# Performance work log

Measured on AMD Instinct MI355X. Metric: run time of the kernel, lower is better.

Reference implementation:

```python
import jax, jax.numpy as jnp
import numpy as np

NHEAD = 16

def setup_inputs() -> dict:
    key = jax.random.key(0)
    ks = jax.random.split(key, 5)
    B, S, D = 4, 2048, 1024
    x = jax.random.normal(ks[0], (B, S, D), dtype=jnp.float32)
    in_proj_weight = jax.random.normal(ks[1], (3 * D, D), dtype=jnp.float32) * (D ** -0.5)
    in_proj_bias = jax.random.normal(ks[2], (3 * D,), dtype=jnp.float32) * 0.02
    out_w = jax.random.normal(ks[3], (D, D), dtype=jnp.float32) * (D ** -0.5)
    out_b = jax.random.normal(ks[4], (D,), dtype=jnp.float32) * 0.02
    return {"x": x, "in_proj_weight": in_proj_weight, "in_proj_bias": in_proj_bias,
            "out_w": out_w, "out_b": out_b}

def reference(x, in_proj_weight, in_proj_bias, out_w, out_b):
    # Faithful to nn.MultiheadAttention self-attn (prefill path, no mask).
    B, S, D = x.shape
    H = NHEAD
    hd = D // H
    qkv = x @ in_proj_weight.T + in_proj_bias            # [B,S,3D]
    q, k, v = jnp.split(qkv, 3, axis=-1)                 # each [B,S,D]
    def heads(t):
        return t.reshape(B, S, H, hd).transpose(0, 2, 1, 3)  # [B,H,S,hd]
    q, k, v = heads(q), heads(k), heads(v)
    scale = hd ** -0.5
    scores = jnp.einsum('bhqd,bhkd->bhqk', q * scale, k)  # [B,H,S,S]
    attn = jax.nn.softmax(scores, axis=-1)
    o = jnp.einsum('bhqk,bhkd->bhqd', attn, v)            # [B,H,S,hd]
    o = o.transpose(0, 2, 1, 3).reshape(B, S, D)
    return o @ out_w.T + out_b
```

## Files before the change

kernel.cpp:

```cpp
#include <hip/hip_runtime.h>
#include <hip/hip_bf16.h>
#include <math.h>

typedef __bf16 bf16_t;
typedef __bf16 bf16x8 __attribute__((ext_vector_type(8)));
typedef float  f32x4  __attribute__((ext_vector_type(4)));

#define DEV __device__ __forceinline__

#define BSZ    4
#define SEQ    2048
#define DMODEL 1024
#define NHEADS 16
#define HDIM   64
#define MROWS  (BSZ*SEQ)
#define KDIM   1024
#define NQKV   (3*DMODEL)

#define GLOAD_LDS16(src, dst)                                                  \
  __builtin_amdgcn_global_load_lds(                                            \
      (__attribute__((address_space(1))) void*)(void*)(src),                   \
      (__attribute__((address_space(3))) void*)(dst), 16, 0, 0)

DEV unsigned cvtpk_bf16(float lo, float hi) {
  unsigned r;
  asm("v_cvt_pk_bf16_f32 %0, %1, %2" : "=v"(r) : "v"(lo), "v"(hi));
  return r;
}

__global__ void cast3_f32_to_bf16(const float* __restrict__ a, int na4,
                                  const float* __restrict__ b, int nb4,
                                  const float* __restrict__ c, int nc4,
                                  bf16_t* __restrict__ oa,
                                  bf16_t* __restrict__ ob,
                                  bf16_t* __restrict__ oc) {
  union U { bf16_t h[4]; uint2 u; };
  int total = na4 + nb4 + nc4;
  for (int i = blockIdx.x * blockDim.x + threadIdx.x; i < total;
       i += gridDim.x * blockDim.x) {
    const float* src; bf16_t* dst; int k;
    if (i < na4)            { src = a; dst = oa; k = i; }
    else if (i < na4 + nb4) { src = b; dst = ob; k = i - na4; }
    else                    { src = c; dst = oc; k = i - na4 - nb4; }
    float4 v = reinterpret_cast<const float4*>(src)[k];
    U r;
    r.h[0] = (bf16_t)v.x; r.h[1] = (bf16_t)v.y;
    r.h[2] = (bf16_t)v.z; r.h[3] = (bf16_t)v.w;
    reinterpret_cast<uint2*>(dst)[k] = r.u;
  }
}

DEV void gemm_tile(const bf16_t* __restrict__ A, const bf16_t* __restrict__ Bt,
                   int row0, int col0, char* smem, f32x4 acc[4][4]) {
  const int t    = threadIdx.x;
  const int lane = t & 63;
  const int wid  = t >> 6;
  const int wm   = (wid >> 1) * 64;
  const int wn   = (wid & 1) * 64;
  const int l15  = lane & 15;
  const int lhi  = lane >> 4;

  char* As = smem;
  char* Bs = smem + 16384;

  const f32x4 fzero = {0.f, 0.f, 0.f, 0.f};
#pragma unroll
  for (int mi = 0; mi < 4; mi++)
#pragma unroll
    for (int ni = 0; ni < 4; ni++) acc[mi][ni] = fzero;

  const char* Abase = (const char*)A;
  const char* Bbase = (const char*)Bt;

  for (int k0 = 0; k0 < KDIM; k0 += 64) {
    __syncthreads();
#pragma unroll
    for (int i = 0; i < 4; i++) {
      int o   = (t + i * 256) * 16;
      int row = o >> 7;
      int cbs = (o & 127) ^ ((row & 7) << 4);
      GLOAD_LDS16(Abase + ((size_t)(row0 + row) * KDIM + k0) * 2 + cbs, As + o);
      GLOAD_LDS16(Bbase + ((size_t)(col0 + row) * KDIM + k0) * 2 + cbs, Bs + o);
    }
    __syncthreads();

#pragma unroll
    for (int ks = 0; ks < 2; ks++) {
      bf16x8 a[4], b[4];
      int byt = ks * 64 + lhi * 16;
#pragma unroll
      for (int mi = 0; mi < 4; mi++) {
        int r = wm + mi * 16 + l15;
        a[mi] = *(const bf16x8*)(As + r * 128 + (byt ^ ((r & 7) << 4)));
      }
#pragma unroll
      for (int ni = 0; ni < 4; ni++) {
        int r = wn + ni * 16 + l15;
        b[ni] = *(const bf16x8*)(Bs + r * 128 + (byt ^ ((r & 7) << 4)));
      }
#pragma unroll
      for (int mi = 0; mi < 4; mi++)
#pragma unroll
        for (int ni = 0; ni < 4; ni++)
          acc[mi][ni] = __builtin_amdgcn_mfma_f32_16x16x32_bf16(
              a[mi], b[ni], acc[mi][ni], 0, 0, 0);
    }
  }
}

__global__ void gemm_qkv_kernel(const bf16_t* __restrict__ xb,
                                const bf16_t* __restrict__ wqkv,
                                const float* __restrict__ bias,
                                bf16_t* __restrict__ Qg, bf16_t* __restrict__ Kg,
                                bf16_t* __restrict__ Vt) {
  __shared__ char smem[34816];
  f32x4 acc[4][4];
  const int bx = blockIdx.x;
  const int wg = (bx & 7) * 192 + (bx >> 3);
  const int mt = wg / 24, nt = wg % 24;
  const int row0 = mt * 128, col0 = nt * 128;
  gemm_tile(xb, wqkv, row0, col0, smem, acc);

  const int t = threadIdx.x, lane = t & 63, wid = t >> 6;
  const int wm = (wid >> 1) * 64, wn = (wid & 1) * 64;
  const int l15 = lane & 15, lhi = lane >> 4;
  const float qscale = 0.125f * 1.44269504f;

  if (nt < 16) {
#pragma unroll
    for (int mi = 0; mi < 4; mi++)
#pragma unroll
      for (int ni = 0; ni < 4; ni++)
#pragma unroll
        for (int j = 0; j < 4; j++) {
          int m = row0 + wm + mi * 16 + lhi * 4 + j;
          int n = col0 + wn + ni * 16 + l15;
          float v = acc[mi][ni][j] + bias[n];
          int b = m >> 11, s = m & 2047;
          int which = n >> 10, rem = n & 1023;
          int h = rem >> 6, d = rem & 63;
          size_t bh = (size_t)(b * NHEADS + h);
          if (which == 0) {
            Qg[(bh * SEQ + s) * HDIM + d] = (bf16_t)(v * qscale);
          } else {
            Kg[(bh * SEQ + s) * HDIM + d] = (bf16_t)v;
          }
        }
  } else {
    __syncthreads();
#pragma unroll
    for (int mi = 0; mi < 4; mi++)
#pragma unroll
      for (int ni = 0; ni < 4; ni++) {
        int nl = wn + ni * 16 + l15;
        int n  = col0 + nl;
        float bi = bias[n];
        int mbase = wm + mi * 16 + lhi * 4;
        float v0 = acc[mi][ni][0] + bi, v1 = acc[mi][ni][1] + bi;
        float v2 = acc[mi][ni][2] + bi, v3 = acc[mi][ni][3] + bi;
        *(unsigned*)(smem + nl * 272 + mbase * 2)     = cvtpk_bf16(v0, v1);
        *(unsigned*)(smem + nl * 272 + mbase * 2 + 4) = cvtpk_bf16(v2, v3);
      }
    __syncthreads();
    const int b  = row0 >> 11, s0 = row0 & 2047;
    const int hbase = (col0 - 2048) >> 6;
#pragma unroll
    for (int it = 0; it < 8; it++) {
      int idx = it * 256 + t;
      int nl = idx >> 4, T = (idx >> 3) & 1, c = idx & 7;
      const char* rb = smem + nl * 272 + T * 128 + 4 * c;
      unsigned r0 = *(const unsigned*)(rb);
      unsigned r1 = *(const unsigned*)(rb + 32);
      unsigned r2 = *(const unsigned*)(rb + 64);
      unsigned r3 = *(const unsigned*)(rb + 96);
      uint4 o;
      o.x = (r0 & 0xffffu) | (r1 << 16);
      o.y = (r2 & 0xffffu) | (r3 << 16);
      o.z = (r0 >> 16) | (r1 & 0xffff0000u);
      o.w = (r2 >> 16) | (r3 & 0xffff0000u);
      int h = hbase + (nl >> 6), d = nl & 63;
      size_t elem = ((size_t)(b * NHEADS + h) * HDIM + d) * SEQ +
                    (size_t)(s0 + T * 64 + 8 * c);
      *(uint4*)((char*)Vt + elem * 2) = o;
    }
  }
}

__global__ void gemm_out_kernel(const bf16_t* __restrict__ Og,
                                const bf16_t* __restrict__ wo,
                                const float* __restrict__ bias,
                                float* __restrict__ out) {
  __shared__ char smem[32768];
  f32x4 acc[4][4];
  const int bx = blockIdx.x;
  const int wg = (bx & 7) * 64 + (bx >> 3);
  const int mt = wg >> 3, nt = wg & 7;
  const int row0 = mt * 128, col0 = nt * 128;
  gemm_tile(Og, wo, row0, col0, smem, acc);

  const int t = threadIdx.x, lane = t & 63, wid = t >> 6;
  const int wm = (wid >> 1) * 64, wn = (wid & 1) * 64;
  const int l15 = lane & 15, lhi = lane >> 4;
#pragma unroll
  for (int mi = 0; mi < 4; mi++)
#pragma unroll
    for (int ni = 0; ni < 4; ni++)
#pragma unroll
      for (int j = 0; j < 4; j++) {
        int m = row0 + wm + mi * 16 + lhi * 4 + j;
        int n = col0 + wn + ni * 16 + l15;
        out[(size_t)m * DMODEL + n] = acc[mi][ni][j] + bias[n];
      }
}

__global__ __launch_bounds__(512, 2)
void attn_kernel(const bf16_t* __restrict__ Qg,
                 const bf16_t* __restrict__ Kg,
                 const bf16_t* __restrict__ Vt,
                 bf16_t* __restrict__ Og) {
  __shared__ char smem[65536];
  char* Ps = smem + 32768;

  const int t = threadIdx.x, lane = t & 63, w = t >> 6;
  const int l15 = lane & 15, lhi = lane >> 4;
  char* Pw = Ps + w * 4096;

  const int xcd = blockIdx.x & 7, slot = blockIdx.x >> 3;
  const int bh = xcd * 8 + (slot >> 3), qt = slot & 7;

  const char* Kb = (const char*)Kg + (size_t)bh * SEQ * HDIM * 2;
  const char* Vb = (const char*)Vt + (size_t)bh * HDIM * SEQ * 2;

  const int so = t * 16;
  const int srow = so >> 7;
  const int scbs = (so & 127) ^ ((srow & 7) << 4);
  const char* gK = Kb + (size_t)srow * 128 + scbs;
  const char* gV = Vb + (size_t)srow * 4096 + scbs;

  const int swz = (l15 & 7) << 4;
  const int koff0 = l15 * 128 + ((lhi * 16) ^ swz);
  const int koff1 = l15 * 128 + ((64 + lhi * 16) ^ swz);
  int woff[4];
#pragma unroll
  for (int j = 0; j < 4; j++)
    woff[j] = (lhi * 4 + j) * 128 + ((8 * l15) ^ (((lhi * 4 + j) & 7) << 4));

  auto STAGE = [&](int buf, int kt) {
    char* Kd = smem + buf * 16384;
    char* Vd = Kd + 8192;
    GLOAD_LDS16(gK + (size_t)kt * 8192, Kd + so);
    GLOAD_LDS16(gV + (size_t)kt * 128, Vd + so);
  };

  STAGE(1, 0);

  bf16x8 qf[2][2];
#pragma unroll
  for (int mi = 0; mi < 2; mi++)
#pragma unroll
    for (int ks = 0; ks < 2; ks++) {
      int q = qt * 256 + w * 32 + mi * 16 + l15;
      qf[mi][ks] = *(const bf16x8*)((const char*)Qg +
                   ((size_t)bh * SEQ + q) * 128 + ks * 64 + lhi * 16);
    }

  const f32x4 fzero = {0.f, 0.f, 0.f, 0.f};
  float lpart[2][4];
  f32x4 oacc[2][4];
#pragma unroll
  for (int mi = 0; mi < 2; mi++)
#pragma unroll
    for (int j = 0; j < 4; j++) { lpart[mi][j] = 0.f; oacc[mi][j] = fzero; }

  int cur = 1;
  for (int kt = 0; kt < SEQ / 64; kt++) {
    __syncthreads();
    if (kt < SEQ / 64 - 1) STAGE(cur ^ 1, kt + 1);

    char* Ks = smem + cur * 16384;
    char* Vs = Ks + 8192;

    f32x4 sacc[2][4];
#pragma unroll
    for (int mi = 0; mi < 2; mi++)
#pragma unroll
      for (int ni = 0; ni < 4; ni++) sacc[mi][ni] = fzero;
    __builtin_amdgcn_s_setprio(1);
#pragma unroll
    for (int ks = 0; ks < 2; ks++) {
      const int ko = ks ? koff1 : koff0;
      bf16x8 kf[4];
#pragma unroll
      for (int ni = 0; ni < 4; ni++)
        kf[ni] = *(const bf16x8*)(Ks + ko + ni * 2048);
#pragma unroll
      for (int mi = 0; mi < 2; mi++)
#pragma unroll
        for (int ni = 0; ni < 4; ni++)
          sacc[mi][ni] = __builtin_amdgcn_mfma_f32_16x16x32_bf16(
              qf[mi][ks], kf[ni], sacc[mi][ni], 0, 0, 0);
    }
    __builtin_amdgcn_s_setprio(0);

#pragma unroll
    for (int mi = 0; mi < 2; mi++)
#pragma unroll
      for (int j = 0; j < 4; j++) {
        float p[4];
#pragma unroll
        for (int ni = 0; ni < 4; ni++)
          p[ni] = __builtin_amdgcn_exp2f(sacc[mi][ni][j]);
        lpart[mi][j] += (p[0] + p[1]) + (p[2] + p[3]);
        uint2 pk;
        pk.x = cvtpk_bf16(p[0], p[1]);
        pk.y = cvtpk_bf16(p[2], p[3]);
        *(uint2*)(Pw + mi * 2048 + woff[j]) = pk;
      }

    __builtin_amdgcn_s_setprio(1);
#pragma unroll
    for (int ks = 0; ks < 2; ks++) {
      const int ko = ks ? koff1 : koff0;
      bf16x8 pf[2], vf[4];
#pragma unroll
      for (int mi = 0; mi < 2; mi++)
        pf[mi] = *(const bf16x8*)(Pw + ko + mi * 2048);
#pragma unroll
      for (int db = 0; db < 4; db++)
        vf[db] = *(const bf16x8*)(Vs + ko + db * 2048);
#pragma unroll
      for (int mi = 0; mi < 2; mi++)
#pragma unroll
        for (int db = 0; db < 4; db++)
          oacc[mi][db] = __builtin_amdgcn_mfma_f32_16x16x32_bf16(
              pf[mi], vf[db], oacc[mi][db], 0, 0, 0);
    }
    __builtin_amdgcn_s_setprio(0);
    cur ^= 1;
  }

  float linv[2][4];
#pragma unroll
  for (int mi = 0; mi < 2; mi++)
#pragma unroll
    for (int j = 0; j < 4; j++) {
      float ls = lpart[mi][j];
      ls += __shfl_xor(ls, 1, 64);
      ls += __shfl_xor(ls, 2, 64);
      ls += __shfl_xor(ls, 4, 64);
      ls += __shfl_xor(ls, 8, 64);
      linv[mi][j] = 1.0f / ls;
    }
  const int b = bh >> 4, h = bh & 15;
#pragma unroll
  for (int mi = 0; mi < 2; mi++)
#pragma unroll
    for (int db = 0; db < 4; db++)
#pragma unroll
      for (int j = 0; j < 4; j++) {
        int srow = qt * 256 + w * 32 + mi * 16 + lhi * 4 + j;
        int d = db * 16 + l15;
        float v = oacc[mi][db][j] * linv[mi][j];
        Og[((size_t)b * SEQ + srow) * DMODEL + h * HDIM + d] = (bf16_t)v;
      }
}

extern "C" void kernel_launch(void* const* d_in, const int* in_sizes, int n_in,
                              void* d_out, int out_size, void* d_ws,
                              size_t ws_size, hipStream_t stream) {
  (void)in_sizes; (void)n_in; (void)out_size; (void)ws_size;
  const float* x     = (const float*)d_in[0];
  const float* w_in  = (const float*)d_in[1];
  const float* b_in  = (const float*)d_in[2];
  const float* w_out = (const float*)d_in[3];
  const float* b_out = (const float*)d_in[4];
  float* out = (float*)d_out;

  char* ws = (char*)d_ws;
  bf16_t* xb  = (bf16_t*)ws; ws += (size_t)MROWS * KDIM * 2;
  bf16_t* wqb = (bf16_t*)ws; ws += (size_t)NQKV * KDIM * 2;
  bf16_t* wob = (bf16_t*)ws; ws += (size_t)DMODEL * KDIM * 2;
  bf16_t* Qg  = (bf16_t*)ws; ws += (size_t)MROWS * DMODEL * 2;
  bf16_t* Kg  = (bf16_t*)ws; ws += (size_t)MROWS * DMODEL * 2;
  bf16_t* Vt  = (bf16_t*)ws; ws += (size_t)MROWS * DMODEL * 2;
  bf16_t* Og  = (bf16_t*)ws; ws += (size_t)MROWS * DMODEL * 2;

  cast3_f32_to_bf16<<<2048, 256, 0, stream>>>(
      x, MROWS * KDIM / 4, w_in, NQKV * KDIM / 4, w_out, DMODEL * KDIM / 4,
      xb, wqb, wob);

  gemm_qkv_kernel<<<64 * 24, 256, 0, stream>>>(xb, wqb, b_in, Qg, Kg, Vt);
  attn_kernel<<<512, 512, 0, stream>>>(Qg, Kg, Vt, Og);
  gemm_out_kernel<<<64 * 8, 256, 0, stream>>>(Og, wob, b_out, out);
}
```

Baseline: 161.3 us.

## Widen QKV GEMM tile to 128x256 with 3-stage async LDS pipeline

The QKV projection kernel is rewritten inline rather than calling the shared gemm_tile helper. It now uses 512-thread blocks computing 128x256 output tiles. Operands are staged through a triple-buffered LDS ring filled with direct global-to-LDS loads, with explicit vmcnt waits so the next two K-slices load while the current one is multiplied. Each block reuses more loaded data and overlaps loads with compute, at the cost of 144KB of LDS per block, which limits the kernel to about one block per CU. The epilogue index math is adjusted for the wider tile.

Result: no change. 160.3 us (-0.6%).

```diff
diff --git a/kernel.cpp b/kernel.cpp
--- a/kernel.cpp
+++ b/kernel.cpp
@@ -108,25 +108,92 @@
   }
 }
 
-__global__ void gemm_qkv_kernel(const bf16_t* __restrict__ xb,
-                                const bf16_t* __restrict__ wqkv,
-                                const float* __restrict__ bias,
-                                bf16_t* __restrict__ Qg, bf16_t* __restrict__ Kg,
-                                bf16_t* __restrict__ Vt) {
-  __shared__ char smem[34816];
+__global__ __launch_bounds__(512, 2)
+void gemm_qkv_kernel(const bf16_t* __restrict__ xb,
+                     const bf16_t* __restrict__ wqkv,
+                     const float* __restrict__ bias,
+                     bf16_t* __restrict__ Qg, bf16_t* __restrict__ Kg,
+                     bf16_t* __restrict__ Vt) {
+  __shared__ char smem[147456];
+
+  const int t = threadIdx.x, lane = t & 63, wid = t >> 6;
+  const int l15 = lane & 15, lhi = lane >> 4;
+  const int wm = (wid >> 2) * 64;
+  const int wn = (wid & 3) * 64;
+
+  const int bx = blockIdx.x;
+  const int wg = (bx & 7) * 96 + (bx >> 3);
+  const int mt = wg / 12, nt = wg % 12;
+  const int row0 = mt * 128, col0 = nt * 256;
+
+  const char* Ax = (const char*)xb;
+  const char* Bx = (const char*)wqkv;
+
+  auto STAGE8 = [&](int bf, int u) {
+    char* Ad = smem + bf * 16384;
+    char* Bd = smem + 49152 + bf * 32768;
+    size_t kof = (size_t)u * 128;
+#pragma unroll
+    for (int r = 0; r < 2; r++) {
+      int o = (r * 512 + t) * 16;
+      int row = o >> 7;
+      int cbs = (o & 127) ^ ((row & 7) << 4);
+      GLOAD_LDS16(Ax + (((size_t)(row0 + row)) << 11) + kof + cbs, Ad + o);
+    }
+#pragma unroll
+    for (int r = 0; r < 4; r++) {
+      int o = (r * 512 + t) * 16;
+      int row = o >> 7;
+      int cbs = (o & 127) ^ ((row & 7) << 4);
+      GLOAD_LDS16(Bx + (((size_t)(col0 + row)) << 11) + kof + cbs, Bd + o);
+    }
+  };
+
   f32x4 acc[4][4];
-  const int bx = blockIdx.x;
-  const int wg = (bx & 7) * 192 + (bx >> 3);
-  const int mt = wg / 24, nt = wg % 24;
-  const int row0 = mt * 128, col0 = nt * 128;
-  gemm_tile(xb, wqkv, row0, col0, smem, acc);
-
-  const int t = threadIdx.x, lane = t & 63, wid = t >> 6;
-  const int wm = (wid >> 1) * 64, wn = (wid & 1) * 64;
-  const int l15 = lane & 15, lhi = lane >> 4;
+  const f32x4 fzero = {0.f, 0.f, 0.f, 0.f};
+#pragma unroll
+  for (int mi = 0; mi < 4; mi++)
+#pragma unroll
+    for (int ni = 0; ni < 4; ni++) acc[mi][ni] = fzero;
+
+  STAGE8(0, 0);
+  STAGE8(1, 1);
+
+#pragma unroll
+  for (int u = 0; u < 16; u++) {
+    if (u < 15) asm volatile("s_waitcnt vmcnt(6)" ::: "memory");
+    else        asm volatile("s_waitcnt vmcnt(0)" ::: "memory");
+    __builtin_amdgcn_s_barrier();
+    if (u + 2 < 16) STAGE8((u + 2) % 3, u + 2);
+
+    char* Ab = smem + (u % 3) * 16384;
+    char* Bb = smem + 49152 + (u % 3) * 32768;
+#pragma unroll
+    for (int ks = 0; ks < 2; ks++) {
+      bf16x8 a[4], b[4];
+      int byt = ks * 64 + lhi * 16;
+#pragma unroll
+      for (int mi = 0; mi < 4; mi++) {
+        int r = wm + mi * 16 + l15;
+        a[mi] = *(const bf16x8*)(Ab + r * 128 + (byt ^ ((r & 7) << 4)));
+      }
+#pragma unroll
+      for (int ni = 0; ni < 4; ni++) {
+        int r = wn + ni * 16 + l15;
+        b[ni] = *(const bf16x8*)(Bb + r * 128 + (byt ^ ((r & 7) << 4)));
+      }
+#pragma unroll
+      for (int mi = 0; mi < 4; mi++)
+#pragma unroll
+        for (int ni = 0; ni < 4; ni++)
+          acc[mi][ni] = __builtin_amdgcn_mfma_f32_16x16x32_bf16(
+              a[mi], b[ni], acc[mi][ni], 0, 0, 0);
+    }
+  }
+
   const float qscale = 0.125f * 1.44269504f;
 
-  if (nt < 16) {
+  if (nt < 8) {
 #pragma unroll
     for (int mi = 0; mi < 4; mi++)
 #pragma unroll
@@ -166,7 +233,7 @@
     const int hbase = (col0 - 2048) >> 6;
 #pragma unroll
     for (int it = 0; it < 8; it++) {
-      int idx = it * 256 + t;
+      int idx = it * 512 + t;
       int nl = idx >> 4, T = (idx >> 3) & 1, c = idx & 7;
       const char* rb = smem + nl * 272 + T * 128 + 4 * c;
       unsigned r0 = *(const unsigned*)(rb);
@@ -389,7 +456,7 @@
       x, MROWS * KDIM / 4, w_in, NQKV * KDIM / 4, w_out, DMODEL * KDIM / 4,
       xb, wqb, wob);
 
-  gemm_qkv_kernel<<<64 * 24, 256, 0, stream>>>(xb, wqb, b_in, Qg, Kg, Vt);
+  gemm_qkv_kernel<<<768, 512, 0, stream>>>(xb, wqb, b_in, Qg, Kg, Vt);
   attn_kernel<<<512, 512, 0, stream>>>(Qg, Kg, Vt, Og);
   gemm_out_kernel<<<64 * 8, 256, 0, stream>>>(Og, wob, b_out, out);
 }
```
